# Kernel tuning notes

Hardware: AMD Instinct MI355X
Metric: run time of the kernel (lower is better)

The kernel has to match this reference:

```python
import jax, jax.numpy as jnp
import numpy as np

B, T, C, H = 4096, 128, 128, 64  # T must equal BLOCK_SIZE=128, C=EMBEDDING_DIM=128


def setup_inputs() -> dict:
    key = jax.random.key(0)
    k1, k2, k3, k4, k5, k6 = jax.random.split(key, 6)
    source_embedding = jax.random.normal(k1, (B, T, C), dtype=jnp.float32)
    target_embedding = jax.random.normal(k2, (B, T, C), dtype=jnp.float32)
    # realistic padding: positions < length are valid; guarantees col 0 valid (no NaN rows)
    lengths = jax.random.randint(k3, (B,), 1, T + 1)
    pad_mask = jnp.arange(T)[None, :] < lengths[:, None]  # (B, T) bool
    Wq = jax.random.normal(k4, (C, H), dtype=jnp.float32) * 0.02
    Wk = jax.random.normal(k5, (C, H), dtype=jnp.float32) * 0.02
    Wv = jax.random.normal(k6, (C, H), dtype=jnp.float32) * 0.02
    return {"source_embedding": source_embedding, "target_embedding": target_embedding,
            "pad_mask": pad_mask, "Wq": Wq, "Wk": Wk, "Wv": Wv}


def reference(source_embedding, target_embedding, pad_mask, Wq, Wk, Wv):
    # q from target, k/v from source (cross-attention capable), bias-free projections
    q = target_embedding @ Wq   # (B, T, H)
    k = source_embedding @ Wk   # (B, T, H)
    v = source_embedding @ Wv   # (B, T, H)
    scale = k.shape[-1] ** -0.5
    wei = jnp.einsum('btd,bsd->bts', q, k) * scale  # (B, T, T)
    causal = jnp.tril(jnp.ones((T, T), dtype=bool))  # needs_future_mask=True
    mask = pad_mask[:, None, :] & causal[None, :, :]  # fuse pad + future masks
    wei = jnp.where(mask, wei, -jnp.inf)
    wei = jax.nn.softmax(wei, axis=-1)
    # dropout disabled (eval mode) for deterministic reference
    out = wei @ v  # (B, T, H)
    return out
```

## Files before the change

### kernel.cpp

```cpp
#include <hip/hip_runtime.h>
#include <stdint.h>


typedef uint32_t u32x2 __attribute__((ext_vector_type(2)));
typedef uint32_t u32x4 __attribute__((ext_vector_type(4)));
typedef float    f32x4 __attribute__((ext_vector_type(4)));
typedef __bf16   bf16x8 __attribute__((ext_vector_type(8)));

static __device__ __forceinline__ uint32_t bf16rne(float a) {
  uint32_t u = __builtin_bit_cast(uint32_t, a);
  u += 0x7FFFu + ((u >> 16) & 1u);
  return u >> 16;
}
static __device__ __forceinline__ uint32_t pack2(float a, float b) {
  uint32_t ua = __builtin_bit_cast(uint32_t, a);
  uint32_t ub = __builtin_bit_cast(uint32_t, b);
  ua += 0x7FFFu + ((ua >> 16) & 1u);
  ub += 0x7FFFu + ((ub >> 16) & 1u);
  return (ua >> 16) | (ub & 0xFFFF0000u);
}
static __device__ __forceinline__ f32x4 mfma16(u32x4 a, u32x4 b, f32x4 c) {
  return __builtin_amdgcn_mfma_f32_16x16x32_bf16(
      __builtin_bit_cast(bf16x8, a), __builtin_bit_cast(bf16x8, b), c, 0, 0, 0);
}

__global__ void prep_w(const float* __restrict__ Wq, const float* __restrict__ Wk,
                       const float* __restrict__ Wv, const void* __restrict__ mask,
                       uint32_t* __restrict__ ws) {
  const int blk = blockIdx.x;
  const int l = threadIdx.x;
  if (blk < 48) {
    const int m  = blk >> 4;
    const int ct = (blk >> 2) & 3;
    const int ks = blk & 3;
    const float* W = (m == 0) ? Wq : ((m == 1) ? Wk : Wv);
    const int h  = ct * 16 + (l & 15);
    const int c0 = ks * 32 + (l >> 4) * 8;
    u32x4 v;
#pragma unroll
    for (int p = 0; p < 4; ++p)
      v[p] = pack2(W[(c0 + 2 * p) * 64 + h], W[(c0 + 2 * p + 1) * 64 + h]);
    ((u32x4*)ws)[blk * 64 + l] = v;
  } else {
    const uint32_t* mw = (const uint32_t*)mask;
    int fl = 0;
    for (int i = l * 16; i < l * 16 + 16; ++i) {
      uint32_t x = mw[i];
      if (x == 0x3F800000u) fl = 2;
      else if (x > 1u && fl != 2) fl = 1;
    }
#pragma unroll
    for (int off = 32; off > 0; off >>= 1) {
      int o = __shfl_down(fl, off);
      fl = (o > fl) ? o : fl;
    }
    if (l == 0) ws[12288] = (uint32_t)fl;
  }
}

__global__ __launch_bounds__(512, 4) void attn_fused(
    const float* __restrict__ src, const float* __restrict__ tgt,
    const void* __restrict__ mask, const uint32_t* __restrict__ ws,
    float* __restrict__ out) {
  __shared__ __align__(16) uint8_t lds[66048];
  uint8_t* const EMB = lds;
  uint8_t* const Qb  = lds + 16384;
  uint8_t* const Kb  = lds + 32768;
  uint8_t* const Vb  = lds + 49152;
  float*  const BIAS = (float*)(lds + 65536);

  const int b   = blockIdx.x;
  const int tid = (int)threadIdx.x;
  const int l   = tid & 63;
  const int w   = tid >> 6;
  const int ct4 = w & 3;
  const int l15 = l & 15;
  const int l7  = l & 7;
  const int g4  = l >> 4;

  const u32x4* wsv = (const u32x4*)ws;
  u32x4 wqf[4], wkf[4], wvf[4];
#pragma unroll
  for (int ks = 0; ks < 4; ++ks) {
    wqf[ks] = wsv[((0 * 4 + ct4) * 4 + ks) * 64 + l];
    wkf[ks] = wsv[((1 * 4 + ct4) * 4 + ks) * 64 + l];
    wvf[ks] = wsv[((2 * 4 + ct4) * 4 + ks) * 64 + l];
  }
  const int mflag = (int)ws[12288];

  const float* const srcb = src + (size_t)b * 16384;
  const float* const tgtb = tgt + (size_t)b * 16384;

  const int r_st = tid >> 3;
  const int j_st = tid & 7;
  f32x4 pf0, pf1, pf2, pf3;
  auto stage_load = [&](const float* gbase) {
    const f32x4* g4p = (const f32x4*)(gbase + r_st * 128 + j_st * 16);
    pf0 = g4p[0]; pf1 = g4p[1]; pf2 = g4p[2]; pf3 = g4p[3];
  };
  auto stage_write = [&]() {
    u32x4 c0 = { pack2(pf0[0], pf0[1]), pack2(pf0[2], pf0[3]),
                 pack2(pf1[0], pf1[1]), pack2(pf1[2], pf1[3]) };
    u32x4 c1 = { pack2(pf2[0], pf2[1]), pack2(pf2[2], pf2[3]),
                 pack2(pf3[0], pf3[1]), pack2(pf3[2], pf3[3]) };
    const uint32_t rs = (uint32_t)(r_st & 7);
    *(u32x4*)(EMB + (r_st << 8) + ((((uint32_t)(2 * j_st)) ^ rs) << 4))     = c0;
    *(u32x4*)(EMB + (r_st << 8) + ((((uint32_t)(2 * j_st + 1)) ^ rs) << 4)) = c1;
  };

  auto gemm_kv = [&](int half) {
    const int rt0  = (w >> 2) * 2;
    const int rowA = rt0 * 16 + l15;
    const int rowB = rowA + 16;
    f32x4 ak0 = {0,0,0,0}, ak1 = {0,0,0,0}, av0 = {0,0,0,0}, av1 = {0,0,0,0};
#pragma unroll
    for (int ks = 0; ks < 4; ++ks) {
      const uint32_t ch = (uint32_t)(ks * 4 + g4);
      u32x4 aA = *(const u32x4*)(EMB + (rowA << 8) + ((ch ^ (uint32_t)(rowA & 7)) << 4));
      u32x4 aB = *(const u32x4*)(EMB + (rowB << 8) + ((ch ^ (uint32_t)(rowB & 7)) << 4));
      ak0 = mfma16(aA, wkf[ks], ak0);
      ak1 = mfma16(aB, wkf[ks], ak1);
      av0 = mfma16(aA, wvf[ks], av0);
      av1 = mfma16(aB, wvf[ks], av1);
    }
    const int h = ct4 * 16 + l15;
    const uint32_t hch = (uint32_t)(h >> 3);
#pragma unroll
    for (int i = 0; i < 2; ++i) {
      const f32x4 kk = i ? ak1 : ak0;
      const f32x4 vv = i ? av1 : av0;
      const int s0 = half * 64 + (rt0 + i) * 16 + g4 * 4;
#pragma unroll
      for (int r = 0; r < 4; ++r) {
        const int s = s0 + r;
        *(uint16_t*)(Kb + (s << 7) + ((hch ^ (uint32_t)(s & 7)) << 4) + ((h & 7) << 1)) =
            (uint16_t)bf16rne(kk[r]);
      }
      u32x2 vpk = { pack2(vv[0], vv[1]), pack2(vv[2], vv[3]) };
      *(u32x2*)(Vb + (h << 8) + (((uint32_t)(s0 >> 3) ^ (uint32_t)(h & 7)) << 4) +
                ((s0 & 7) << 1)) = vpk;
    }
  };
  auto gemm_q = [&](int half) {
    const int rt0  = (w >> 2) * 2;
    const int rowA = rt0 * 16 + l15;
    const int rowB = rowA + 16;
    f32x4 aq0 = {0,0,0,0}, aq1 = {0,0,0,0};
#pragma unroll
    for (int ks = 0; ks < 4; ++ks) {
      const uint32_t ch = (uint32_t)(ks * 4 + g4);
      u32x4 aA = *(const u32x4*)(EMB + (rowA << 8) + ((ch ^ (uint32_t)(rowA & 7)) << 4));
      u32x4 aB = *(const u32x4*)(EMB + (rowB << 8) + ((ch ^ (uint32_t)(rowB & 7)) << 4));
      aq0 = mfma16(aA, wqf[ks], aq0);
      aq1 = mfma16(aB, wqf[ks], aq1);
    }
    const int h = ct4 * 16 + l15;
    const uint32_t hch = (uint32_t)(h >> 3);
#pragma unroll
    for (int i = 0; i < 2; ++i) {
      const f32x4 qq = i ? aq1 : aq0;
      const int t0 = half * 64 + (rt0 + i) * 16 + g4 * 4;
#pragma unroll
      for (int r = 0; r < 4; ++r) {
        const int t = t0 + r;
        *(uint16_t*)(Qb + (t << 7) + ((hch ^ (uint32_t)(t & 7)) << 4) + ((h & 7) << 1)) =
            (uint16_t)bf16rne(qq[r]);
      }
    }
  };

  stage_load(srcb);
  stage_write();
  if (tid < 128) {
    bool valid;
    if (mflag == 1)      valid = ((const uint8_t*)mask)[b * 128 + tid] != 0;
    else if (mflag == 0) valid = ((const int*)mask)[b * 128 + tid] != 0;
    else                 valid = ((const float*)mask)[b * 128 + tid] != 0.0f;
    BIAS[tid] = valid ? 0.0f : -1e30f;
  }
  __syncthreads();
  stage_load(srcb + 8192);  gemm_kv(0);  __syncthreads();
  stage_write();                          __syncthreads();
  stage_load(tgtb);         gemm_kv(1);  __syncthreads();
  stage_write();                          __syncthreads();
  stage_load(tgtb + 8192);  gemm_q(0);   __syncthreads();
  stage_write();                          __syncthreads();
  gemm_q(1);                             __syncthreads();

  const int qrow = w * 16 + l15;
  u32x4 qa0 = *(const u32x4*)(Qb + (qrow << 7) + ((((uint32_t)g4)      ^ (uint32_t)l7) << 4));
  u32x4 qa1 = *(const u32x4*)(Qb + (qrow << 7) + ((((uint32_t)(4 + g4)) ^ (uint32_t)l7) << 4));

  f32x4 sacc[8];
#pragma unroll
  for (int ct = 0; ct < 8; ++ct) sacc[ct] = {0,0,0,0};
#pragma unroll
  for (int ct = 0; ct < 8; ++ct) {
    const int srow = ct * 16 + l15;
    u32x4 kb0 = *(const u32x4*)(Kb + (srow << 7) + ((((uint32_t)g4)      ^ (uint32_t)l7) << 4));
    u32x4 kb1 = *(const u32x4*)(Kb + (srow << 7) + ((((uint32_t)(4 + g4)) ^ (uint32_t)l7) << 4));
    sacc[ct] = mfma16(qa0, kb0, sacc[ct]);
    sacc[ct] = mfma16(qa1, kb1, sacc[ct]);
  }

  float biasr[8];
#pragma unroll
  for (int ct = 0; ct < 8; ++ct) biasr[ct] = BIAS[ct * 16 + l15];

  float inv[4];
#pragma unroll
  for (int r = 0; r < 4; ++r) {
    const int t = w * 16 + g4 * 4 + r;
    float m = -3.0e38f;
#pragma unroll
    for (int ct = 0; ct < 8; ++ct) {
      const int s = ct * 16 + l15;
      float v = sacc[ct][r] * 0.125f + biasr[ct];
      v = (s <= t) ? v : -1.0e30f;
      sacc[ct][r] = v;
      m = fmaxf(m, v);
    }
    m = fmaxf(m, __shfl_xor(m, 1));
    m = fmaxf(m, __shfl_xor(m, 2));
    m = fmaxf(m, __shfl_xor(m, 4));
    m = fmaxf(m, __shfl_xor(m, 8));
    float sum = 0.0f;
#pragma unroll
    for (int ct = 0; ct < 8; ++ct) {
      float p = __expf(sacc[ct][r] - m);
      sacc[ct][r] = p;
      sum += p;
    }
    sum += __shfl_xor(sum, 1);
    sum += __shfl_xor(sum, 2);
    sum += __shfl_xor(sum, 4);
    sum += __shfl_xor(sum, 8);
    inv[r] = 1.0f / sum;
  }

  __syncthreads();

  uint8_t* const Pw = Qb + (w << 12);
#pragma unroll
  for (int ct = 0; ct < 8; ++ct) {
    const int s = ct * 16 + l15;
    const uint32_t sch = (uint32_t)(s >> 3);
#pragma unroll
    for (int r = 0; r < 4; ++r) {
      const int tl = g4 * 4 + r;
      *(uint16_t*)(Pw + (tl << 8) + ((sch ^ (uint32_t)(tl & 7)) << 4) + ((s & 7) << 1)) =
          (uint16_t)bf16rne(sacc[ct][r]);
    }
  }

  f32x4 oacc[4];
#pragma unroll
  for (int ct = 0; ct < 4; ++ct) oacc[ct] = {0,0,0,0};
#pragma unroll
  for (int ks = 0; ks < 4; ++ks) {
    const uint32_t ch = (uint32_t)(ks * 4 + g4);
    u32x4 pa = *(const u32x4*)(Pw + (l15 << 8) + ((ch ^ (uint32_t)l7) << 4));
#pragma unroll
    for (int ct = 0; ct < 4; ++ct) {
      const int vrow = ct * 16 + l15;
      u32x4 vb = *(const u32x4*)(Vb + (vrow << 8) + ((ch ^ (uint32_t)l7) << 4));
      oacc[ct] = mfma16(pa, vb, oacc[ct]);
    }
  }

  float* const ob = out + (size_t)b * 8192;
#pragma unroll
  for (int ct = 0; ct < 4; ++ct) {
#pragma unroll
    for (int r = 0; r < 4; ++r) {
      const int t = w * 16 + g4 * 4 + r;
      ob[t * 64 + ct * 16 + l15] = oacc[ct][r] * inv[r];
    }
  }
}

extern "C" void kernel_launch(void* const* d_in, const int* in_sizes, int n_in,
                              void* d_out, int out_size, void* d_ws, size_t ws_size,
                              hipStream_t stream) {
  const float* src = (const float*)d_in[0];
  const float* tgt = (const float*)d_in[1];
  const void*  msk = d_in[2];
  const float* Wq  = (const float*)d_in[3];
  const float* Wk  = (const float*)d_in[4];
  const float* Wv  = (const float*)d_in[5];
  uint32_t* ws = (uint32_t*)d_ws;
  float* out = (float*)d_out;
  const int B = in_sizes[0] / (128 * 128);

  hipLaunchKernelGGL(prep_w, dim3(49), dim3(64), 0, stream, Wq, Wk, Wv, msk, ws);
  hipLaunchKernelGGL(attn_fused, dim3(B), dim3(512), 0, stream,
                     src, tgt, msk, ws, out);
}
```

Measured before the change: 153.0 us.

## Transpose MFMA operand roles to vectorize LDS stores and per-lane softmax

Swaps the A/B operands in the projection, score and PV MFMAs so each lane holds a contiguous column of results. This turns scalar 16-bit LDS stores into packed 8-byte stores and lets each lane own one query row, so the softmax needs only two cross-lane shuffles and the output is written as float4. It also coalesces the global staging loads, loads Wq lazily to cut register pressure, and stores P across the EMB/Qb regions behind a barrier. The trade-off is changed swizzle patterns, which could introduce LDS bank conflicts, plus an added barrier before the PV stage.

```diff
diff --git a/kernel.cpp b/kernel.cpp
--- a/kernel.cpp
+++ b/kernel.cpp
@@ -7,11 +7,6 @@
 typedef float    f32x4 __attribute__((ext_vector_type(4)));
 typedef __bf16   bf16x8 __attribute__((ext_vector_type(8)));
 
-static __device__ __forceinline__ uint32_t bf16rne(float a) {
-  uint32_t u = __builtin_bit_cast(uint32_t, a);
-  u += 0x7FFFu + ((u >> 16) & 1u);
-  return u >> 16;
-}
 static __device__ __forceinline__ uint32_t pack2(float a, float b) {
   uint32_t ua = __builtin_bit_cast(uint32_t, a);
   uint32_t ub = __builtin_bit_cast(uint32_t, b);
@@ -73,209 +68,188 @@
   const int tid = (int)threadIdx.x;
   const int l   = tid & 63;
   const int w   = tid >> 6;
-  const int ct4 = w & 3;
   const int l15 = l & 15;
-  const int l7  = l & 7;
   const int g4  = l >> 4;
+  const int ct  = w & 3;
+  const int sg  = (w >> 2) * 2;
 
   const u32x4* wsv = (const u32x4*)ws;
-  u32x4 wqf[4], wkf[4], wvf[4];
-#pragma unroll
-  for (int ks = 0; ks < 4; ++ks) {
-    wqf[ks] = wsv[((0 * 4 + ct4) * 4 + ks) * 64 + l];
-    wkf[ks] = wsv[((1 * 4 + ct4) * 4 + ks) * 64 + l];
-    wvf[ks] = wsv[((2 * 4 + ct4) * 4 + ks) * 64 + l];
-  }
   const int mflag = (int)ws[12288];
-
   const float* const srcb = src + (size_t)b * 16384;
   const float* const tgtb = tgt + (size_t)b * 16384;
 
-  const int r_st = tid >> 3;
-  const int j_st = tid & 7;
-  f32x4 pf0, pf1, pf2, pf3;
+  u32x4 wk[4], wv[4], wq[4];
+#pragma unroll
+  for (int ks = 0; ks < 4; ++ks) {
+    wk[ks] = wsv[((4 + ct) * 4 + ks) * 64 + l];
+    wv[ks] = wsv[((8 + ct) * 4 + ks) * 64 + l];
+  }
+
+  f32x4 pf[4];
   auto stage_load = [&](const float* gbase) {
-    const f32x4* g4p = (const f32x4*)(gbase + r_st * 128 + j_st * 16);
-    pf0 = g4p[0]; pf1 = g4p[1]; pf2 = g4p[2]; pf3 = g4p[3];
+#pragma unroll
+    for (int p = 0; p < 4; ++p)
+      pf[p] = *(const f32x4*)(gbase + tid * 4 + p * 2048);
   };
   auto stage_write = [&]() {
-    u32x4 c0 = { pack2(pf0[0], pf0[1]), pack2(pf0[2], pf0[3]),
-                 pack2(pf1[0], pf1[1]), pack2(pf1[2], pf1[3]) };
-    u32x4 c1 = { pack2(pf2[0], pf2[1]), pack2(pf2[2], pf2[3]),
-                 pack2(pf3[0], pf3[1]), pack2(pf3[2], pf3[3]) };
-    const uint32_t rs = (uint32_t)(r_st & 7);
-    *(u32x4*)(EMB + (r_st << 8) + ((((uint32_t)(2 * j_st)) ^ rs) << 4))     = c0;
-    *(u32x4*)(EMB + (r_st << 8) + ((((uint32_t)(2 * j_st + 1)) ^ rs) << 4)) = c1;
-  };
-
-  auto gemm_kv = [&](int half) {
-    const int rt0  = (w >> 2) * 2;
-    const int rowA = rt0 * 16 + l15;
-    const int rowB = rowA + 16;
-    f32x4 ak0 = {0,0,0,0}, ak1 = {0,0,0,0}, av0 = {0,0,0,0}, av1 = {0,0,0,0};
-#pragma unroll
-    for (int ks = 0; ks < 4; ++ks) {
-      const uint32_t ch = (uint32_t)(ks * 4 + g4);
-      u32x4 aA = *(const u32x4*)(EMB + (rowA << 8) + ((ch ^ (uint32_t)(rowA & 7)) << 4));
-      u32x4 aB = *(const u32x4*)(EMB + (rowB << 8) + ((ch ^ (uint32_t)(rowB & 7)) << 4));
-      ak0 = mfma16(aA, wkf[ks], ak0);
-      ak1 = mfma16(aB, wkf[ks], ak1);
-      av0 = mfma16(aA, wvf[ks], av0);
-      av1 = mfma16(aB, wvf[ks], av1);
-    }
-    const int h = ct4 * 16 + l15;
-    const uint32_t hch = (uint32_t)(h >> 3);
+#pragma unroll
+    for (int p = 0; p < 4; ++p) {
+      const int c   = tid + p * 512;
+      const int row = c >> 5;
+      const int cc  = c & 31;
+      u32x2 d = { pack2(pf[p][0], pf[p][1]), pack2(pf[p][2], pf[p][3]) };
+      *(u32x2*)(EMB + (row << 8) + ((((cc >> 1) ^ (row & 7))) << 4) + ((cc & 1) << 3)) = d;
+    }
+  };
+
+  auto projKV = [&](int half) {
 #pragma unroll
     for (int i = 0; i < 2; ++i) {
-      const f32x4 kk = i ? ak1 : ak0;
-      const f32x4 vv = i ? av1 : av0;
-      const int s0 = half * 64 + (rt0 + i) * 16 + g4 * 4;
-#pragma unroll
-      for (int r = 0; r < 4; ++r) {
-        const int s = s0 + r;
-        *(uint16_t*)(Kb + (s << 7) + ((hch ^ (uint32_t)(s & 7)) << 4) + ((h & 7) << 1)) =
-            (uint16_t)bf16rne(kk[r]);
+      const int st  = sg + i;
+      const int row = st * 16 + l15;
+      f32x4 cK = {0, 0, 0, 0}, cV = {0, 0, 0, 0};
+#pragma unroll
+      for (int ks = 0; ks < 4; ++ks) {
+        u32x4 e = *(const u32x4*)(EMB + (row << 8) + ((((ks * 4 + g4) ^ (row & 7))) << 4));
+        cK = mfma16(wk[ks], e, cK);
+        cV = mfma16(e, wv[ks], cV);
       }
-      u32x2 vpk = { pack2(vv[0], vv[1]), pack2(vv[2], vv[3]) };
-      *(u32x2*)(Vb + (h << 8) + (((uint32_t)(s0 >> 3) ^ (uint32_t)(h & 7)) << 4) +
-                ((s0 & 7) << 1)) = vpk;
-    }
-  };
-  auto gemm_q = [&](int half) {
-    const int rt0  = (w >> 2) * 2;
-    const int rowA = rt0 * 16 + l15;
-    const int rowB = rowA + 16;
-    f32x4 aq0 = {0,0,0,0}, aq1 = {0,0,0,0};
-#pragma unroll
-    for (int ks = 0; ks < 4; ++ks) {
-      const uint32_t ch = (uint32_t)(ks * 4 + g4);
-      u32x4 aA = *(const u32x4*)(EMB + (rowA << 8) + ((ch ^ (uint32_t)(rowA & 7)) << 4));
-      u32x4 aB = *(const u32x4*)(EMB + (rowB << 8) + ((ch ^ (uint32_t)(rowB & 7)) << 4));
-      aq0 = mfma16(aA, wqf[ks], aq0);
-      aq1 = mfma16(aB, wqf[ks], aq1);
-    }
-    const int h = ct4 * 16 + l15;
-    const uint32_t hch = (uint32_t)(h >> 3);
+      const int s  = half * 64 + st * 16 + l15;
+      const int h0 = ct * 16 + g4 * 4;
+      u32x2 dk = { pack2(cK[0], cK[1]), pack2(cK[2], cK[3]) };
+      *(u32x2*)(Kb + (s << 7) + ((((h0 >> 3) ^ (s & 7))) << 4) + ((h0 & 7) << 1)) = dk;
+      const int s0 = half * 64 + st * 16 + g4 * 4;
+      const int h  = ct * 16 + l15;
+      u32x2 dv = { pack2(cV[0], cV[1]), pack2(cV[2], cV[3]) };
+      *(u32x2*)(Vb + (h << 8) + ((((s0 >> 3) ^ (h & 7))) << 4) + ((s0 & 7) << 1)) = dv;
+    }
+  };
+  auto projQ = [&](int half) {
 #pragma unroll
     for (int i = 0; i < 2; ++i) {
-      const f32x4 qq = i ? aq1 : aq0;
-      const int t0 = half * 64 + (rt0 + i) * 16 + g4 * 4;
-#pragma unroll
-      for (int r = 0; r < 4; ++r) {
-        const int t = t0 + r;
-        *(uint16_t*)(Qb + (t << 7) + ((hch ^ (uint32_t)(t & 7)) << 4) + ((h & 7) << 1)) =
-            (uint16_t)bf16rne(qq[r]);
+      const int st  = sg + i;
+      const int row = st * 16 + l15;
+      f32x4 cQ = {0, 0, 0, 0};
+#pragma unroll
+      for (int ks = 0; ks < 4; ++ks) {
+        u32x4 e = *(const u32x4*)(EMB + (row << 8) + ((((ks * 4 + g4) ^ (row & 7))) << 4));
+        cQ = mfma16(wq[ks], e, cQ);
       }
+      const int t  = half * 64 + st * 16 + l15;
+      const int h0 = ct * 16 + g4 * 4;
+      u32x2 dq = { pack2(cQ[0], cQ[1]), pack2(cQ[2], cQ[3]) };
+      *(u32x2*)(Qb + (t << 7) + ((((h0 >> 3) ^ (t & 7))) << 4) + ((h0 & 7) << 1)) = dq;
     }
   };
 
   stage_load(srcb);
-  stage_write();
+  float biasv = 0.0f;
   if (tid < 128) {
     bool valid;
     if (mflag == 1)      valid = ((const uint8_t*)mask)[b * 128 + tid] != 0;
     else if (mflag == 0) valid = ((const int*)mask)[b * 128 + tid] != 0;
     else                 valid = ((const float*)mask)[b * 128 + tid] != 0.0f;
-    BIAS[tid] = valid ? 0.0f : -1e30f;
-  }
-  __syncthreads();
-  stage_load(srcb + 8192);  gemm_kv(0);  __syncthreads();
-  stage_write();                          __syncthreads();
-  stage_load(tgtb);         gemm_kv(1);  __syncthreads();
-  stage_write();                          __syncthreads();
-  stage_load(tgtb + 8192);  gemm_q(0);   __syncthreads();
-  stage_write();                          __syncthreads();
-  gemm_q(1);                             __syncthreads();
-
-  const int qrow = w * 16 + l15;
-  u32x4 qa0 = *(const u32x4*)(Qb + (qrow << 7) + ((((uint32_t)g4)      ^ (uint32_t)l7) << 4));
-  u32x4 qa1 = *(const u32x4*)(Qb + (qrow << 7) + ((((uint32_t)(4 + g4)) ^ (uint32_t)l7) << 4));
+    biasv = valid ? 0.0f : -1e30f;
+  }
+  stage_write();
+  if (tid < 128) BIAS[tid] = biasv;
+  __syncthreads();
+  stage_load(srcb + 8192);
+  projKV(0);
+  __syncthreads();
+  stage_write();
+  __syncthreads();
+  stage_load(tgtb);
+  projKV(1);
+#pragma unroll
+  for (int ks = 0; ks < 4; ++ks)
+    wq[ks] = wsv[(ct * 4 + ks) * 64 + l];
+  __syncthreads();
+  stage_write();
+  __syncthreads();
+  stage_load(tgtb + 8192);
+  projQ(0);
+  __syncthreads();
+  stage_write();
+  __syncthreads();
+  projQ(1);
+  __syncthreads();
+
+  const int tq = 16 * w + l15;
+  u32x4 qf0 = *(const u32x4*)(Qb + (tq << 7) + (((g4 ^ (tq & 7))) << 4));
+  u32x4 qf1 = *(const u32x4*)(Qb + (tq << 7) + ((((4 + g4) ^ (tq & 7))) << 4));
 
   f32x4 sacc[8];
 #pragma unroll
-  for (int ct = 0; ct < 8; ++ct) sacc[ct] = {0,0,0,0};
-#pragma unroll
-  for (int ct = 0; ct < 8; ++ct) {
-    const int srow = ct * 16 + l15;
-    u32x4 kb0 = *(const u32x4*)(Kb + (srow << 7) + ((((uint32_t)g4)      ^ (uint32_t)l7) << 4));
-    u32x4 kb1 = *(const u32x4*)(Kb + (srow << 7) + ((((uint32_t)(4 + g4)) ^ (uint32_t)l7) << 4));
-    sacc[ct] = mfma16(qa0, kb0, sacc[ct]);
-    sacc[ct] = mfma16(qa1, kb1, sacc[ct]);
-  }
-
-  float biasr[8];
-#pragma unroll
-  for (int ct = 0; ct < 8; ++ct) biasr[ct] = BIAS[ct * 16 + l15];
-
-  float inv[4];
-#pragma unroll
-  for (int r = 0; r < 4; ++r) {
-    const int t = w * 16 + g4 * 4 + r;
-    float m = -3.0e38f;
-#pragma unroll
-    for (int ct = 0; ct < 8; ++ct) {
-      const int s = ct * 16 + l15;
-      float v = sacc[ct][r] * 0.125f + biasr[ct];
-      v = (s <= t) ? v : -1.0e30f;
-      sacc[ct][r] = v;
+  for (int mt = 0; mt < 8; ++mt) sacc[mt] = {0, 0, 0, 0};
+#pragma unroll
+  for (int mt = 0; mt < 8; ++mt) {
+    const int srow = mt * 16 + l15;
+    u32x4 k0 = *(const u32x4*)(Kb + (srow << 7) + (((g4 ^ (srow & 7))) << 4));
+    u32x4 k1 = *(const u32x4*)(Kb + (srow << 7) + ((((4 + g4) ^ (srow & 7))) << 4));
+    sacc[mt] = mfma16(k0, qf0, sacc[mt]);
+    sacc[mt] = mfma16(k1, qf1, sacc[mt]);
+  }
+
+  float m = -3.0e38f;
+#pragma unroll
+  for (int mt = 0; mt < 8; ++mt) {
+    f32x4 b4 = *(const f32x4*)(BIAS + mt * 16 + g4 * 4);
+#pragma unroll
+    for (int r = 0; r < 4; ++r) {
+      float v = sacc[mt][r] * 0.125f + b4[r];
+      sacc[mt][r] = v;
       m = fmaxf(m, v);
     }
-    m = fmaxf(m, __shfl_xor(m, 1));
-    m = fmaxf(m, __shfl_xor(m, 2));
-    m = fmaxf(m, __shfl_xor(m, 4));
-    m = fmaxf(m, __shfl_xor(m, 8));
-    float sum = 0.0f;
-#pragma unroll
-    for (int ct = 0; ct < 8; ++ct) {
-      float p = __expf(sacc[ct][r] - m);
-      sacc[ct][r] = p;
+  }
+  m = fmaxf(m, __shfl_xor(m, 16));
+  m = fmaxf(m, __shfl_xor(m, 32));
+  float sum = 0.0f;
+#pragma unroll
+  for (int mt = 0; mt < 8; ++mt) {
+#pragma unroll
+    for (int r = 0; r < 4; ++r) {
+      const int s = mt * 16 + g4 * 4 + r;
+      float p = __expf(sacc[mt][r] - m);
+      p = (s <= tq) ? p : 0.0f;
+      sacc[mt][r] = p;
       sum += p;
     }
-    sum += __shfl_xor(sum, 1);
-    sum += __shfl_xor(sum, 2);
-    sum += __shfl_xor(sum, 4);
-    sum += __shfl_xor(sum, 8);
-    inv[r] = 1.0f / sum;
-  }
-
-  __syncthreads();
-
-  uint8_t* const Pw = Qb + (w << 12);
-#pragma unroll
-  for (int ct = 0; ct < 8; ++ct) {
-    const int s = ct * 16 + l15;
-    const uint32_t sch = (uint32_t)(s >> 3);
-#pragma unroll
-    for (int r = 0; r < 4; ++r) {
-      const int tl = g4 * 4 + r;
-      *(uint16_t*)(Pw + (tl << 8) + ((sch ^ (uint32_t)(tl & 7)) << 4) + ((s & 7) << 1)) =
-          (uint16_t)bf16rne(sacc[ct][r]);
-    }
-  }
+  }
+  sum += __shfl_xor(sum, 16);
+  sum += __shfl_xor(sum, 32);
+  const float inv = 1.0f / sum;
+
+  uint8_t* const Pr = (l15 < 8) ? (EMB + w * 2048 + l15 * 256)
+                                : (Qb + w * 2048 + (l15 - 8) * 256);
+#pragma unroll
+  for (int mt = 0; mt < 8; ++mt) {
+    u32x2 d = { pack2(sacc[mt][0], sacc[mt][1]), pack2(sacc[mt][2], sacc[mt][3]) };
+    const int c = mt * 2 + (g4 >> 1);
+    *(u32x2*)(Pr + (((c ^ l15)) << 4) + ((g4 & 1) << 3)) = d;
+  }
+  __syncthreads();
 
   f32x4 oacc[4];
 #pragma unroll
-  for (int ct = 0; ct < 4; ++ct) oacc[ct] = {0,0,0,0};
+  for (int vt = 0; vt < 4; ++vt) oacc[vt] = {0, 0, 0, 0};
 #pragma unroll
   for (int ks = 0; ks < 4; ++ks) {
-    const uint32_t ch = (uint32_t)(ks * 4 + g4);
-    u32x4 pa = *(const u32x4*)(Pw + (l15 << 8) + ((ch ^ (uint32_t)l7) << 4));
-#pragma unroll
-    for (int ct = 0; ct < 4; ++ct) {
-      const int vrow = ct * 16 + l15;
-      u32x4 vb = *(const u32x4*)(Vb + (vrow << 8) + ((ch ^ (uint32_t)l7) << 4));
-      oacc[ct] = mfma16(pa, vb, oacc[ct]);
-    }
-  }
-
-  float* const ob = out + (size_t)b * 8192;
-#pragma unroll
-  for (int ct = 0; ct < 4; ++ct) {
-#pragma unroll
-    for (int r = 0; r < 4; ++r) {
-      const int t = w * 16 + g4 * 4 + r;
-      ob[t * 64 + ct * 16 + l15] = oacc[ct][r] * inv[r];
-    }
+    u32x4 pb = *(const u32x4*)(Pr + ((((ks * 4 + g4) ^ l15)) << 4));
+#pragma unroll
+    for (int vt = 0; vt < 4; ++vt) {
+      const int vrow = vt * 16 + l15;
+      u32x4 vf = *(const u32x4*)(Vb + (vrow << 8) + ((((ks * 4 + g4) ^ (vrow & 7))) << 4));
+      oacc[vt] = mfma16(vf, pb, oacc[vt]);
+    }
+  }
+
+  float* const ob = out + (size_t)b * 8192 + (size_t)tq * 64;
+#pragma unroll
+  for (int vt = 0; vt < 4; ++vt) {
+    f32x4 o = { oacc[vt][0] * inv, oacc[vt][1] * inv,
+                oacc[vt][2] * inv, oacc[vt][3] * inv };
+    *(f32x4*)(ob + vt * 16 + g4 * 4) = o;
   }
 }
 
```

After: 144.8 us. 5.3% less time.
